# Kernel optimization log

Hardware: AMD Instinct MI355X
Metric: run time of the kernel (lower is better)

The kernel has to match this reference:

```python
import jax, jax.numpy as jnp
import numpy as np

G, S, D, H, E = 8, 2048, 1024, 4096, 8  # groups, group_size, d_model, ffn_hidden, experts


def setup_inputs() -> dict:
    key = jax.random.key(0)
    ks = jax.random.split(key, 6)
    s = 0.02
    return {
        "x": jax.random.normal(ks[0], (G, S, D), dtype=jnp.float32),
        "gate_w": jax.random.normal(ks[1], (D, E), dtype=jnp.float32) * s,
        "ew1": jax.random.normal(ks[2], (E, D, H), dtype=jnp.float32) * s,
        "eb1": jnp.zeros((E, H), dtype=jnp.float32),
        "ew2": jax.random.normal(ks[3], (E, H, D), dtype=jnp.float32) * s,
        "eb2": jnp.zeros((E, D), dtype=jnp.float32),
        "sw1": jax.random.normal(ks[4], (D, H), dtype=jnp.float32) * s,
        "sb1": jnp.zeros((H,), dtype=jnp.float32),
        "sw2": jax.random.normal(ks[5], (H, D), dtype=jnp.float32) * s,
        "sb2": jnp.zeros((D,), dtype=jnp.float32),
        "expert_capacity": 2048,
    }


def reference(x, gate_w, ew1, eb1, ew2, eb2, sw1, sb1, sw2, sb2, expert_capacity):
    g, s_, d = x.shape
    e = gate_w.shape[1]
    T = g * s_
    cap = int(expert_capacity)

    # ---- Router (inference path) ----
    router_logits = jnp.einsum('gsd,de->gse', x, gate_w)           # (G,S,E)
    router_probs = jax.nn.softmax(router_logits, axis=-1)
    flat_probs = router_probs.transpose(2, 0, 1).reshape(e, T)      # (E,T)
    pad_w = max(0, cap - T)
    if pad_w > 0:
        flat_probs = jnp.pad(flat_probs, ((0, 0), (0, pad_w)),
                             mode='constant', constant_values=-1e9)
    scores, token_indices = jax.lax.top_k(flat_probs, k=cap)        # (E,C)
    scores = jnp.where(scores > -1e8, scores, 0.0)

    # ---- Routed experts: gather -> grouped FFN -> scale -> scatter-add ----
    x_flat = x.reshape(T, d)                                        # (T,D)
    safe_idx = jnp.clip(token_indices, 0, T - 1)                    # guard padded slots
    toks = x_flat[safe_idx]                                         # (E,C,D)
    h = jax.nn.gelu(jnp.einsum('ecd,edh->ech', toks, ew1) + eb1[:, None, :])
    y = jnp.einsum('ech,ehd->ecd', h, ew2) + eb2[:, None, :]        # (E,C,D)
    y = y * scores[..., None]                                       # zero weight kills padded slots
    routed = jnp.zeros_like(x_flat).at[safe_idx.reshape(-1)].add(y.reshape(-1, d))

    # ---- Shared expert over all tokens ----
    shared = jax.nn.gelu(x_flat @ sw1 + sb1) @ sw2 + sb2            # (T,D)

    return (routed + shared).reshape(g, s_, d)
```

## Files before the change

kernel.cpp:

```cpp
#include <hip/hip_runtime.h>

typedef __bf16 bf16;
typedef __bf16 bf16x8 __attribute__((ext_vector_type(8)));
typedef float f32x4 __attribute__((ext_vector_type(4)));

#define NTOK 16384
#define DMODEL 1024
#define HFFN 4096
#define NEXP 8
#define CAP 2048

#define VMCNT(n) asm volatile("s_waitcnt vmcnt(" #n ")" ::: "memory")
#define BARRIER() __builtin_amdgcn_s_barrier()
#define PRIO1() __builtin_amdgcn_s_setprio(1)
#define PRIO0() __builtin_amdgcn_s_setprio(0)

__device__ __forceinline__ void gload16(const void* g, void* l) {
  __builtin_amdgcn_global_load_lds((const __attribute__((address_space(1))) void*)g,
                                   (__attribute__((address_space(3))) void*)l, 16, 0, 0);
}

__device__ __forceinline__ float gelu_f(float v) {
  float t = v * v;
  float s2 = v * fmaf(0.10294358f, t, 2.3022084f);
  float e = __builtin_exp2f(-s2);
  return v * __builtin_amdgcn_rcpf(1.0f + e);
}

__device__ __forceinline__ void xcd_remap(int& bx, int& by) {
  const int gx = gridDim.x;
  const int lg = 31 - __clz((unsigned)gx);
  const int w = blockIdx.x + gx * blockIdx.y;
  bx = (w >> 3) & (gx - 1);
  by = (w & 7) | (((w >> 3) >> lg) << 3);
}

__global__ __launch_bounds__(256) void cvt_x_kernel(const float* __restrict__ x,
                                                    bf16* __restrict__ xb) {
  int i = blockIdx.x * blockDim.x + threadIdx.x;
  const float4* a = (const float4*)x + (size_t)i * 2;
  float4 v0 = a[0], v1 = a[1];
  bf16x8 o;
  o[0]=(bf16)v0.x; o[1]=(bf16)v0.y; o[2]=(bf16)v0.z; o[3]=(bf16)v0.w;
  o[4]=(bf16)v1.x; o[5]=(bf16)v1.y; o[6]=(bf16)v1.z; o[7]=(bf16)v1.w;
  *(bf16x8*)(xb + (size_t)i * 8) = o;
}

__global__ __launch_bounds__(64) void router_kernel(const float* __restrict__ x,
                                                    const float* __restrict__ gw,
                                                    float* __restrict__ probs) {
  int t = blockIdx.x;
  int l = threadIdx.x;
  int e = l & 7, chunk = l >> 3;
  const float* xr = x + (size_t)t * DMODEL + chunk * 128;
  const float* gwr = gw + (size_t)(chunk * 128) * NEXP + e;
  float a0 = 0.f, a1 = 0.f;
  #pragma unroll
  for (int d = 0; d < 128; d += 8) {
    float4 xv = *(const float4*)(xr + d);
    float4 xw = *(const float4*)(xr + d + 4);
    a0 += xv.x * gwr[(d+0)*8] + xv.y * gwr[(d+1)*8] + xv.z * gwr[(d+2)*8] + xv.w * gwr[(d+3)*8];
    a1 += xw.x * gwr[(d+4)*8] + xw.y * gwr[(d+5)*8] + xw.z * gwr[(d+6)*8] + xw.w * gwr[(d+7)*8];
  }
  float acc = a0 + a1;
  acc += __shfl_xor(acc, 8);
  acc += __shfl_xor(acc, 16);
  acc += __shfl_xor(acc, 32);
  float m = acc;
  m = fmaxf(m, __shfl_xor(m, 1));
  m = fmaxf(m, __shfl_xor(m, 2));
  m = fmaxf(m, __shfl_xor(m, 4));
  float ex = expf(acc - m);
  float s = ex;
  s += __shfl_xor(s, 1); s += __shfl_xor(s, 2); s += __shfl_xor(s, 4);
  if (l < 8) probs[(size_t)e * NTOK + t] = ex / s;
}

__global__ __launch_bounds__(256) void topk_kernel(const float* __restrict__ probs,
                                                   int* __restrict__ oidx,
                                                   float* __restrict__ oscr) {
  const int e = blockIdx.x;
  const float* p = probs + (size_t)e * NTOK;
  const int t = threadIdx.x;
  __shared__ unsigned hist[256];
  __shared__ unsigned sg[256], sq[256];
  __shared__ unsigned bcast[4];
  unsigned pref = 0, krem = CAP;
  for (int pass = 0; pass < 4; ++pass) {
    const int sh = 24 - pass * 8;
    hist[t] = 0;
    __syncthreads();
    for (int j = 0; j < 64; ++j) {
      unsigned u = __float_as_uint(p[t * 64 + j]);
      bool ok = (pass == 0) || ((u >> (sh + 8)) == pref);
      if (ok) atomicAdd(&hist[(u >> sh) & 255u], 1u);
    }
    __syncthreads();
    if (t == 0) {
      unsigned cum = 0; int b = 255;
      for (; b > 0; --b) {
        unsigned c = hist[b];
        if (cum + c >= krem) break;
        cum += c;
      }
      bcast[0] = (pref << 8) | (unsigned)b;
      bcast[1] = krem - cum;
    }
    __syncthreads();
    pref = bcast[0];
    krem = bcast[1];
  }
  const unsigned thr = pref;
  const unsigned neq_take = krem;
  unsigned cgt = 0, ceq = 0;
  for (int j = 0; j < 64; ++j) {
    unsigned u = __float_as_uint(p[t * 64 + j]);
    cgt += (u > thr);
    ceq += (u == thr);
  }
  sg[t] = cgt; sq[t] = ceq;
  __syncthreads();
  if (t == 0) {
    unsigned ag = 0, aq = 0;
    for (int i = 0; i < 256; ++i) {
      unsigned g = sg[i], q = sq[i];
      sg[i] = ag; sq[i] = aq;
      ag += g; aq += q;
    }
    bcast[2] = ag;
  }
  __syncthreads();
  const unsigned ngt = bcast[2];
  unsigned og = sg[t], oq = sq[t];
  int* oi = oidx + e * CAP;
  float* os = oscr + e * CAP;
  for (int j = 0; j < 64; ++j) {
    int tok = t * 64 + j;
    float pv = p[tok];
    unsigned u = __float_as_uint(pv);
    if (u > thr) {
      oi[og] = tok; os[og] = pv; ++og;
    } else if (u == thr) {
      if (oq < neq_take) { oi[ngt + oq] = tok; os[ngt + oq] = pv; }
      ++oq;
    }
  }
}

__global__ __launch_bounds__(256) void transpose_cvt(const float* __restrict__ in_e,
                                                     const float* __restrict__ in_s,
                                                     bf16* __restrict__ outp,
                                                     int R, int C) {
  int z = blockIdx.z;
  const float* in = (z < 8) ? (in_e + (size_t)z * (size_t)R * C) : in_s;
  bf16* out = outp + (size_t)z * (size_t)R * C;
  __shared__ float tile[64][65];
  int tx = threadIdx.x & 63, ty = threadIdx.x >> 6;
  int c0 = blockIdx.x * 64, r0 = blockIdx.y * 64;
  #pragma unroll
  for (int j = 0; j < 16; ++j) {
    int r = ty + j * 4;
    tile[r][tx] = in[(size_t)(r0 + r) * C + c0 + tx];
  }
  __syncthreads();
  #pragma unroll
  for (int j = 0; j < 16; ++j) {
    int c = ty + j * 4;
    out[(size_t)(c0 + c) * R + r0 + tx] = (bf16)tile[tx][c];
  }
}


#define STG_ALO(D, ko) { gload16(srcA0 + (ko), (D) + tid8); gload16(srcA2 + (ko), (D) + 4096 + tid8); }
#define STG_AHI(D, ko) { gload16(srcA1 + (ko), (D) + 8192 + tid8); gload16(srcA3 + (ko), (D) + 12288 + tid8); }
#define STG_BLO(D, ko) { gload16(srcBlo0 + (ko), (D) + 16384 + tid8); gload16(srcBlo1 + (ko), (D) + 20480 + tid8); }
#define STG_BHI(D, ko) { gload16(srcBhi0 + (ko), (D) + 24576 + tid8); gload16(srcBhi1 + (ko), (D) + 28672 + tid8); }

#define RD_A(ARR, D, OFF) \
  _Pragma("unroll") for (int i = 0; i < 4; ++i) { \
    ARR[2*i]   = *(const bf16x8*)((D) + (OFF) + (wr*64 + i*16 + fr)*64 + c0s); \
    ARR[2*i+1] = *(const bf16x8*)((D) + (OFF) + (wr*64 + i*16 + fr)*64 + c1s); \
  }
#define RD_B(ARR, D, OFF) \
  _Pragma("unroll") for (int j = 0; j < 2; ++j) { \
    ARR[2*j]   = *(const bf16x8*)((D) + (OFF) + (wc*32 + j*16 + fr)*64 + c0s); \
    ARR[2*j+1] = *(const bf16x8*)((D) + (OFF) + (wc*32 + j*16 + fr)*64 + c1s); \
  }

#define MFMA_Q(I0, J0, A, B) \
  _Pragma("unroll") for (int i = 0; i < 4; ++i) \
    _Pragma("unroll") for (int j = 0; j < 2; ++j) { \
      acc[(I0)+i][(J0)+j] = __builtin_amdgcn_mfma_f32_16x16x32_bf16((A)[2*i],   (B)[2*j],   acc[(I0)+i][(J0)+j], 0, 0, 0); \
      acc[(I0)+i][(J0)+j] = __builtin_amdgcn_mfma_f32_16x16x32_bf16((A)[2*i+1], (B)[2*j+1], acc[(I0)+i][(J0)+j], 0, 0, 0); \
    }

#define KLOOP(NT) do { \
  bf16* B0_ = smem; \
  bf16* B1_ = smem + 32768; \
  STG_ALO(B0_, 0); STG_BHI(B0_, 0); STG_AHI(B0_, 0); STG_BLO(B0_, 0); \
  VMCNT(0); \
  BARRIER(); \
  RD_B(S1, B0_, 16384); \
  STG_BLO(B1_, 64); STG_ALO(B1_, 64); STG_BHI(B1_, 64); \
  for (int t = 0; t < (NT); t += 2) { \
    const bool st = (t + 2) < (NT); \
    const int ko1 = (t+1)*64, ko2 = (t+2)*64, ko3 = (t+3)*64; \
     \
    RD_A(aA, B0_, 0); \
    STG_AHI(B1_, ko1); \
    BARRIER(); \
    PRIO1(); MFMA_Q(0,0,aA,S1); PRIO0(); \
    BARRIER(); \
     \
    RD_B(S2, B0_, 24576); \
    if (st) STG_BLO(B0_, ko2); \
    BARRIER(); \
    PRIO1(); MFMA_Q(0,2,aA,S2); PRIO0(); \
    BARRIER(); \
     \
    RD_A(aA, B0_, 8192); \
    if (st) STG_ALO(B0_, ko2); \
    BARRIER(); \
    PRIO1(); MFMA_Q(4,2,aA,S2); PRIO0(); \
    BARRIER(); \
     \
    if (st) { STG_BHI(B0_, ko2); VMCNT(6); } else { VMCNT(0); } \
    RD_B(S2, B1_, 16384); \
    BARRIER(); \
    PRIO1(); MFMA_Q(4,0,aA,S1); PRIO0(); \
    BARRIER(); \
     \
    RD_A(aA, B1_, 0); \
    if (st) STG_AHI(B0_, ko2); \
    BARRIER(); \
    PRIO1(); MFMA_Q(0,0,aA,S2); PRIO0(); \
    BARRIER(); \
     \
    RD_B(S1, B1_, 24576); \
    if (st) STG_BLO(B1_, ko3); \
    BARRIER(); \
    PRIO1(); MFMA_Q(0,2,aA,S1); PRIO0(); \
    BARRIER(); \
     \
    RD_A(aA, B1_, 8192); \
    if (st) STG_ALO(B1_, ko3); \
    BARRIER(); \
    PRIO1(); MFMA_Q(4,2,aA,S1); PRIO0(); \
    BARRIER(); \
     \
    if (st) { STG_BHI(B1_, ko3); VMCNT(6); RD_B(S1, B0_, 16384); } \
    else { VMCNT(0); } \
    BARRIER(); \
    PRIO1(); MFMA_Q(4,0,aA,S2); PRIO0(); \
    BARRIER(); \
  } \
} while (0)

__global__ __launch_bounds__(512, 2) void ffn1_gemm(const bf16* __restrict__ xb,
                                                    const bf16* __restrict__ w1t,
                                                    const float* __restrict__ bias1,
                                                    const int* __restrict__ sel,
                                                    bf16* __restrict__ hout,
                                                    int routed) {
  const int e = blockIdx.z;
  const bf16* Bw = w1t + (routed ? (size_t)e * HFFN * DMODEL : 0);
  const float* bias = bias1 + (routed ? (size_t)e * HFFN : 0);
  bf16* hb = hout + (routed ? (size_t)e * CAP * HFFN : 0);
  int bx, by;
  xcd_remap(bx, by);
  const int m0 = by * 256, n0 = bx * 256;
  __shared__ __align__(16) bf16 smem[65536];
  const int tid = threadIdx.x, lane = tid & 63, wave = tid >> 6;
  const int wr = wave >> 2, wc = wave & 3;
  const int tid8 = tid * 8;

  const int p = tid >> 3, sch = tid & 7;
  const int schs = sch ^ (p & 7);
  const int brow = p + (p & 32);
  const bf16 *srcA0, *srcA1, *srcA2, *srcA3, *srcBlo0, *srcBlo1, *srcBhi0, *srcBhi1;
  {
    int ra0 = routed ? sel[e * CAP + m0 + p]       : (m0 + p);
    int ra1 = routed ? sel[e * CAP + m0 + 64 + p]  : (m0 + 64 + p);
    int ra2 = routed ? sel[e * CAP + m0 + 128 + p] : (m0 + 128 + p);
    int ra3 = routed ? sel[e * CAP + m0 + 192 + p] : (m0 + 192 + p);
    srcA0 = xb + (size_t)ra0 * DMODEL + schs * 8;
    srcA1 = xb + (size_t)ra1 * DMODEL + schs * 8;
    srcA2 = xb + (size_t)ra2 * DMODEL + schs * 8;
    srcA3 = xb + (size_t)ra3 * DMODEL + schs * 8;
    srcBlo0 = Bw + (size_t)(n0 + brow) * DMODEL + schs * 8;
    srcBlo1 = srcBlo0 + (size_t)128 * DMODEL;
    srcBhi0 = srcBlo0 + (size_t)32 * DMODEL;
    srcBhi1 = srcBlo0 + (size_t)160 * DMODEL;
  }

  f32x4 acc[8][4];
  #pragma unroll
  for (int i = 0; i < 8; ++i)
    #pragma unroll
    for (int j = 0; j < 4; ++j) acc[i][j] = (f32x4){0.f, 0.f, 0.f, 0.f};

  const int fr = lane & 15;
  const int k8 = lane >> 4;
  const int sw = lane & 7;
  const int c0s = (k8 ^ sw) * 8;
  const int c1s = ((k8 + 4) ^ sw) * 8;
  bf16x8 aA[8], S1[4], S2[4];

  KLOOP(DMODEL / 64);

  __syncthreads();
  #pragma unroll
  for (int half = 0; half < 2; ++half) {
    if (wr == half) {
      #pragma unroll
      for (int i = 0; i < 8; ++i) {
        #pragma unroll
        for (int j = 0; j < 4; ++j) {
          const int nl = wc * 64 + j * 16 + fr;
          const float bb = bias[n0 + nl];
          #pragma unroll
          for (int q = 0; q < 4; ++q) {
            const int ml = i * 16 + (lane >> 4) * 4 + q;
            smem[ml * 256 + (nl ^ (((ml >> 2) & 7) << 4))] =
                (bf16)gelu_f(acc[i][j][q] + bb);
          }
        }
      }
    }
    __syncthreads();
    #pragma unroll
    for (int pp = 0; pp < 8; ++pp) {
      const int flat = pp * 512 + tid;
      const int row = flat >> 5, nc8 = flat & 31;
      uint4 v = *(const uint4*)(smem + row * 256 + ((nc8 * 8) ^ (((row >> 2) & 7) << 4)));
      *(uint4*)(hb + (size_t)(m0 + half * 128 + row) * HFFN + n0 + nc8 * 8) = v;
    }
    __syncthreads();
  }
}

__global__ __launch_bounds__(512, 2) void ffn2_gemm(const bf16* __restrict__ hbuf,
                                                    const bf16* __restrict__ w2t,
                                                    const float* __restrict__ bias2,
                                                    const int* __restrict__ sel,
                                                    const float* __restrict__ scr,
                                                    float* __restrict__ out,
                                                    int routed) {
  const int e = blockIdx.z;
  const bf16* Ab = hbuf + (routed ? (size_t)e * CAP * HFFN : 0);
  const bf16* Bw = w2t + (routed ? (size_t)e * DMODEL * HFFN : 0);
  const float* bias = bias2 + (routed ? (size_t)e * DMODEL : 0);
  int bx, by;
  xcd_remap(bx, by);
  const int m0 = by * 256, n0 = bx * 256;
  __shared__ __align__(16) bf16 smem[65536];
  __shared__ int s_tok[256];
  __shared__ float s_scl[256];
  const int tid = threadIdx.x, lane = tid & 63, wave = tid >> 6;
  const int wr = wave >> 2, wc = wave & 3;
  const int tid8 = tid * 8;

  const int p = tid >> 3, sch = tid & 7;
  const int schs = sch ^ (p & 7);
  const int brow = p + (p & 32);
  const bf16* srcA0 = Ab + (size_t)(m0 + p) * HFFN + schs * 8;
  const bf16* srcA1 = Ab + (size_t)(m0 + 64 + p) * HFFN + schs * 8;
  const bf16* srcA2 = Ab + (size_t)(m0 + 128 + p) * HFFN + schs * 8;
  const bf16* srcA3 = Ab + (size_t)(m0 + 192 + p) * HFFN + schs * 8;
  const bf16* srcBlo0 = Bw + (size_t)(n0 + brow) * HFFN + schs * 8;
  const bf16* srcBlo1 = srcBlo0 + (size_t)128 * HFFN;
  const bf16* srcBhi0 = srcBlo0 + (size_t)32 * HFFN;
  const bf16* srcBhi1 = srcBlo0 + (size_t)160 * HFFN;
  if (routed && tid < 256) {
    s_tok[tid] = sel[e * CAP + m0 + tid];
    s_scl[tid] = scr[e * CAP + m0 + tid];
  }

  f32x4 acc[8][4];
  #pragma unroll
  for (int i = 0; i < 8; ++i)
    #pragma unroll
    for (int j = 0; j < 4; ++j) acc[i][j] = (f32x4){0.f, 0.f, 0.f, 0.f};

  const int fr = lane & 15;
  const int k8 = lane >> 4;
  const int sw = lane & 7;
  const int c0s = (k8 ^ sw) * 8;
  const int c1s = ((k8 + 4) ^ sw) * 8;
  bf16x8 aA[8], S1[4], S2[4];

  KLOOP(HFFN / 64);

  if (!routed) {
    #pragma unroll
    for (int i = 0; i < 8; ++i) {
      #pragma unroll
      for (int j = 0; j < 4; ++j) {
        const int nl = wc * 64 + j * 16 + fr;
        const float bb = bias[n0 + nl];
        #pragma unroll
        for (int q = 0; q < 4; ++q) {
          const int ml = wr * 128 + i * 16 + (lane >> 4) * 4 + q;
          out[(size_t)(m0 + ml) * DMODEL + n0 + nl] = acc[i][j][q] + bb;
        }
      }
    }
  } else {
    __syncthreads();
    #pragma unroll
    for (int i = 0; i < 8; ++i) {
      #pragma unroll
      for (int j = 0; j < 4; ++j) {
        const int nl = wc * 64 + j * 16 + fr;
        const float bb = bias[n0 + nl];
        #pragma unroll
        for (int q = 0; q < 4; ++q) {
          const int ml = wr * 128 + i * 16 + (lane >> 4) * 4 + q;
          const int tok = s_tok[ml];
          const float sc = s_scl[ml];
          atomicAdd(out + (size_t)tok * DMODEL + n0 + nl, (acc[i][j][q] + bb) * sc);
        }
      }
    }
  }
}

extern "C" void kernel_launch(void* const* d_in, const int* in_sizes, int n_in,
                              void* d_out, int out_size, void* d_ws, size_t ws_size,
                              hipStream_t stream) {
  const float* x   = (const float*)d_in[0];
  const float* gw  = (const float*)d_in[1];
  const float* ew1 = (const float*)d_in[2];
  const float* eb1 = (const float*)d_in[3];
  const float* ew2 = (const float*)d_in[4];
  const float* eb2 = (const float*)d_in[5];
  const float* sw1 = (const float*)d_in[6];
  const float* sb1 = (const float*)d_in[7];
  const float* sw2 = (const float*)d_in[8];
  const float* sb2 = (const float*)d_in[9];
  float* out = (float*)d_out;

  char* ws = (char*)d_ws;
  size_t off = 0;
  bf16* xb      = (bf16*)(ws + off); off += (size_t)NTOK * DMODEL * 2;
  bf16* w1t     = (bf16*)(ws + off); off += (size_t)9 * HFFN * DMODEL * 2;
  bf16* w2t     = (bf16*)(ws + off); off += (size_t)9 * DMODEL * HFFN * 2;
  bf16* hbuf    = (bf16*)(ws + off); off += (size_t)NTOK * HFFN * 2;
  float* probs  = (float*)(ws + off); off += (size_t)NEXP * NTOK * 4;
  int* selidx   = (int*)(ws + off);   off += (size_t)NEXP * CAP * 4;
  float* selscr = (float*)(ws + off); off += (size_t)NEXP * CAP * 4;

  cvt_x_kernel<<<dim3(NTOK * DMODEL / 8 / 256), dim3(256), 0, stream>>>(x, xb);
  router_kernel<<<dim3(NTOK), dim3(64), 0, stream>>>(x, gw, probs);
  topk_kernel<<<dim3(NEXP), dim3(256), 0, stream>>>(probs, selidx, selscr);
  transpose_cvt<<<dim3(HFFN / 64, DMODEL / 64, 9), dim3(256), 0, stream>>>(ew1, sw1, w1t, DMODEL, HFFN);
  transpose_cvt<<<dim3(DMODEL / 64, HFFN / 64, 9), dim3(256), 0, stream>>>(ew2, sw2, w2t, HFFN, DMODEL);

  ffn1_gemm<<<dim3(HFFN / 256, NTOK / 256, 1), dim3(512), 0, stream>>>(
      xb, w1t + (size_t)8 * HFFN * DMODEL, sb1, (const int*)nullptr, hbuf, 0);
  ffn2_gemm<<<dim3(DMODEL / 256, NTOK / 256, 1), dim3(512), 0, stream>>>(
      hbuf, w2t + (size_t)8 * DMODEL * HFFN, sb2, (const int*)nullptr, (const float*)nullptr, out, 0);

  ffn1_gemm<<<dim3(HFFN / 256, CAP / 256, NEXP), dim3(512), 0, stream>>>(
      xb, w1t, eb1, selidx, hbuf, 1);
  ffn2_gemm<<<dim3(DMODEL / 256, CAP / 256, NEXP), dim3(512), 0, stream>>>(
      hbuf, w2t, eb2, selidx, selscr, out, 1);
}
```

Measured before the change: 850.9 us.

## Restructure GEMM K-loop into single-stage double-buffered pipeline with fewer barriers

```diff
diff --git a/kernel.cpp b/kernel.cpp
--- a/kernel.cpp
+++ b/kernel.cpp
@@ -197,61 +197,30 @@
 #define KLOOP(NT) do { \
   bf16* B0_ = smem; \
   bf16* B1_ = smem + 32768; \
-  STG_ALO(B0_, 0); STG_BHI(B0_, 0); STG_AHI(B0_, 0); STG_BLO(B0_, 0); \
-  VMCNT(0); \
+  STG_ALO(B0_, 0); STG_AHI(B0_, 0); STG_BLO(B0_, 0); STG_BHI(B0_, 0); \
+  STG_ALO(B1_, 64); STG_BLO(B1_, 64); STG_BHI(B1_, 64); \
+  VMCNT(6); \
   BARRIER(); \
-  RD_B(S1, B0_, 16384); \
-  STG_BLO(B1_, 64); STG_ALO(B1_, 64); STG_BHI(B1_, 64); \
-  for (int t = 0; t < (NT); t += 2) { \
-    const bool st = (t + 2) < (NT); \
-    const int ko1 = (t+1)*64, ko2 = (t+2)*64, ko3 = (t+3)*64; \
+  for (int t = 0; t < (NT); ++t) { \
+    bf16* cur = smem + ((t & 1) << 15); \
+    bf16* nxt = smem + (((t + 1) & 1) << 15); \
+    const int ko1 = (t + 1) * 64, ko2 = (t + 2) * 64; \
+    const bool st1 = (t + 1) < (NT), st2 = (t + 2) < (NT); \
+    bf16x8 aA[8], S1[4], S2[4]; \
      \
-    RD_A(aA, B0_, 0); \
-    STG_AHI(B1_, ko1); \
+    RD_A(aA, cur, 0); \
+    RD_B(S1, cur, 16384); \
+    RD_B(S2, cur, 24576); \
+    if (st1) STG_AHI(nxt, ko1); \
     BARRIER(); \
-    PRIO1(); MFMA_Q(0,0,aA,S1); PRIO0(); \
+    PRIO1(); MFMA_Q(0,0,aA,S1); MFMA_Q(0,2,aA,S2); PRIO0(); \
+     \
+    RD_A(aA, cur, 8192); \
     BARRIER(); \
      \
-    RD_B(S2, B0_, 24576); \
-    if (st) STG_BLO(B0_, ko2); \
-    BARRIER(); \
-    PRIO1(); MFMA_Q(0,2,aA,S2); PRIO0(); \
-    BARRIER(); \
-     \
-    RD_A(aA, B0_, 8192); \
-    if (st) STG_ALO(B0_, ko2); \
-    BARRIER(); \
-    PRIO1(); MFMA_Q(4,2,aA,S2); PRIO0(); \
-    BARRIER(); \
-     \
-    if (st) { STG_BHI(B0_, ko2); VMCNT(6); } else { VMCNT(0); } \
-    RD_B(S2, B1_, 16384); \
-    BARRIER(); \
-    PRIO1(); MFMA_Q(4,0,aA,S1); PRIO0(); \
-    BARRIER(); \
-     \
-    RD_A(aA, B1_, 0); \
-    if (st) STG_AHI(B0_, ko2); \
-    BARRIER(); \
-    PRIO1(); MFMA_Q(0,0,aA,S2); PRIO0(); \
-    BARRIER(); \
-     \
-    RD_B(S1, B1_, 24576); \
-    if (st) STG_BLO(B1_, ko3); \
-    BARRIER(); \
-    PRIO1(); MFMA_Q(0,2,aA,S1); PRIO0(); \
-    BARRIER(); \
-     \
-    RD_A(aA, B1_, 8192); \
-    if (st) STG_ALO(B1_, ko3); \
-    BARRIER(); \
-    PRIO1(); MFMA_Q(4,2,aA,S1); PRIO0(); \
-    BARRIER(); \
-     \
-    if (st) { STG_BHI(B1_, ko3); VMCNT(6); RD_B(S1, B0_, 16384); } \
-    else { VMCNT(0); } \
-    BARRIER(); \
-    PRIO1(); MFMA_Q(4,0,aA,S2); PRIO0(); \
+    if (st2) { STG_ALO(cur, ko2); STG_BLO(cur, ko2); STG_BHI(cur, ko2); } \
+    PRIO1(); MFMA_Q(4,0,aA,S1); MFMA_Q(4,2,aA,S2); PRIO0(); \
+    if (st2) { VMCNT(6); } else { VMCNT(0); } \
     BARRIER(); \
   } \
 } while (0)
@@ -304,7 +273,6 @@
   const int sw = lane & 7;
   const int c0s = (k8 ^ sw) * 8;
   const int c1s = ((k8 + 4) ^ sw) * 8;
-  bf16x8 aA[8], S1[4], S2[4];
 
   KLOOP(DMODEL / 64);
 
@@ -387,7 +355,6 @@
   const int sw = lane & 7;
   const int c0s = (k8 ^ sw) * 8;
   const int c1s = ((k8 + 4) ^ sw) * 8;
-  bf16x8 aA[8], S1[4], S2[4];
 
   KLOOP(HFFN / 64);
 
```

New measurement: 835.8 us. Within noise of the previous version (-1.8%).
